# Kernel tuning notes

Measured on AMD Instinct MI355X. Metric: run time of the kernel, lower is better.

## Reference

```python
import jax, jax.numpy as jnp
import numpy as np
from jax import lax

EPS = 1e-6
NUM_BANDS = 128


def setup_inputs() -> dict:
    key = jax.random.key(0)
    kx, = jax.random.split(key, 1)
    B, C, F, T = 32, 1, NUM_BANDS, 6000
    x = jax.random.uniform(kx, (B, C, F, T), dtype=jnp.float32)  # nonneg spectrogram energies
    # parameters per band, initialized as in PCEN.__init__ (s=0.025, alpha=delta=r=1.0)
    log_s = jnp.full((F,), np.log(0.025), dtype=jnp.float32)
    log_alpha = jnp.zeros((F,), dtype=jnp.float32)
    log_delta = jnp.zeros((F,), dtype=jnp.float32)
    log_r = jnp.zeros((F,), dtype=jnp.float32)
    return {"x": x, "log_s": log_s, "log_alpha": log_alpha,
            "log_delta": log_delta, "log_r": log_r}


def _pcen(x, log_s, log_alpha, log_delta, log_r):
    # x: (B, C, bands, T)
    s = jnp.exp(log_s)  # (bands,)
    xt = jnp.moveaxis(x, -1, 0)  # (T, B, C, bands) time-major for the scan
    init = xt[0]  # init_smoother_from_data=True -> M_0 = X_0

    def step(m, xf):
        m_new = (1.0 - s) * m + s * xf
        return m_new, m_new

    _, ms = lax.scan(step, init, xt[1:])  # (T-1, B, C, bands)
    smoother = jnp.concatenate([init[None], ms], axis=0)  # (T, B, C, bands)
    smoother = jnp.moveaxis(smoother, 0, -1)  # (B, C, bands, T)

    alpha = jnp.exp(log_alpha)[:, None]  # (bands, 1)
    delta = jnp.exp(log_delta)[:, None]
    r = jnp.exp(log_r)[:, None]
    # (eps + M)^(-alpha) computed stably: exp(-alpha * (log eps + log1p(M/eps)))
    gain = jnp.exp(-alpha * (jnp.log(EPS) + jnp.log1p(smoother / EPS)))
    return (x * gain + delta) ** r - delta ** r


def reference(x, log_s, log_alpha, log_delta, log_r):
    return _pcen(x, log_s, log_alpha, log_delta, log_r)
```

## Files before the change

kernel.cpp:

```cpp
#include <hip/hip_runtime.h>

#define TLEN     6000
#define NV4      1500
#define CHUNK_V4 256
#define SUB_V4   64
#define NCHUNK   6
#define EPS      1e-6f
#define LN_EPS   (-13.815511f)
#define INV_EPS  1e6f

__device__ __forceinline__ float pcen_full(float xv, float M, float alpha,
                                           float delta, float r, float deltar) {
    float gain = __expf(-alpha * (LN_EPS + __logf(fmaf(M, INV_EPS, 1.0f))));
    return __powf(fmaf(xv, gain, delta), r) - deltar;
}

__device__ __forceinline__ float ipow6(float b, int e) {
    float r = 1.0f;
    #pragma unroll
    for (int i = 0; i < 6; ++i) {
        if (e & 1) r *= b;
        b *= b;
        e >>= 1;
    }
    return r;
}

template<bool PARTIAL>
__device__ __forceinline__ float chunk_compute(
    const float4 (&q)[4], const int cb, const int lane, const bool finit,
    const float s, const float oms, const float oms4, const float Apow4,
    const float A256, const bool triv,
    const float la, const float ld, const float lr,
    float Mc, float4* __restrict__ ob)
{
    float B[4];
    #pragma unroll
    for (int j = 0; j < 4; ++j) {
        const float c0 = (finit && j == 0 && lane == 0) ? 1.0f : s;
        float b = c0 * q[j].x;
        b = fmaf(oms, b, s * q[j].y);
        b = fmaf(oms, b, s * q[j].z);
        b = fmaf(oms, b, s * q[j].w);
        B[j] = b;
    }

    float S[4];
    #pragma unroll
    for (int j = 0; j < 4; ++j) S[j] = B[j];
    float w = oms4;
    #pragma unroll
    for (int off = 1; off < 64; off <<= 1) {
        #pragma unroll
        for (int j = 0; j < 4; ++j) {
            const float Sp = __shfl_up(S[j], off, 64);
            if (lane >= off) S[j] = fmaf(w, Sp, S[j]);
        }
        w *= w;
    }

    float Min[4];
    #pragma unroll
    for (int j = 0; j < 4; ++j) {
        const float Se = __shfl_up(S[j], 1, 64);
        const float Be = (lane == 0) ? 0.0f : Se;
        Min[j] = fmaf(Apow4, Mc, Be);
        Mc = fmaf(A256, Mc, __shfl(S[j], 63, 64));
    }

    if (triv) {
        #pragma unroll
        for (int j = 0; j < 4; ++j) {
            const int vi = cb + SUB_V4 * j + lane;
            if (!PARTIAL || vi < NV4) {
                const float c0 = (finit && j == 0 && lane == 0) ? 1.0f : s;
                float m = Min[j]; float4 o;
                m = fmaf(oms, m, c0 * q[j].x); o.x = q[j].x * __builtin_amdgcn_rcpf(m + EPS);
                m = fmaf(oms, m, s  * q[j].y); o.y = q[j].y * __builtin_amdgcn_rcpf(m + EPS);
                m = fmaf(oms, m, s  * q[j].z); o.z = q[j].z * __builtin_amdgcn_rcpf(m + EPS);
                m = fmaf(oms, m, s  * q[j].w); o.w = q[j].w * __builtin_amdgcn_rcpf(m + EPS);
                ob[vi] = o;
            }
        }
    } else {
        const float alpha  = __expf(la);
        const float delta  = __expf(ld);
        const float r      = __expf(lr);
        const float deltar = __powf(delta, lr == 0.0f ? 1.0f : r);
        #pragma unroll
        for (int j = 0; j < 4; ++j) {
            const int vi = cb + SUB_V4 * j + lane;
            if (!PARTIAL || vi < NV4) {
                const float c0 = (finit && j == 0 && lane == 0) ? 1.0f : s;
                float m = Min[j]; float4 o;
                m = fmaf(oms, m, c0 * q[j].x); o.x = pcen_full(q[j].x, m, alpha, delta, r, deltar);
                m = fmaf(oms, m, s  * q[j].y); o.y = pcen_full(q[j].y, m, alpha, delta, r, deltar);
                m = fmaf(oms, m, s  * q[j].z); o.z = pcen_full(q[j].z, m, alpha, delta, r, deltar);
                m = fmaf(oms, m, s  * q[j].w); o.w = pcen_full(q[j].w, m, alpha, delta, r, deltar);
                ob[vi] = o;
            }
        }
    }
    return Mc;
}

__global__ __launch_bounds__(256, 4) void pcen_kernel(
    const float* __restrict__ x,
    const float* __restrict__ log_s,
    const float* __restrict__ log_alpha,
    const float* __restrict__ log_delta,
    const float* __restrict__ log_r,
    float* __restrict__ out,
    int num_series, int F)
{
    const int g    = (int)((blockIdx.x * blockDim.x + threadIdx.x) >> 6);
    const int lane = (int)(threadIdx.x & 63);
    if (g >= num_series) return;
    const int series = g;
    const int f      = series % F;

    const float la = log_alpha[f], ld = log_delta[f], lr = log_r[f];
    const bool  triv = (la == 0.0f) && (ld == 0.0f) && (lr == 0.0f);

    const float s    = __expf(log_s[f]);
    const float oms  = 1.0f - s;
    const float oms2 = oms * oms;
    const float oms4 = oms2 * oms2;

    float A256 = oms4;
    #pragma unroll
    for (int i = 0; i < 6; ++i) A256 *= A256;

    const float Apow4 = ipow6(oms4, lane);

    const float4* __restrict__ xb = (const float4*)(x + (size_t)series * TLEN);
    float4* __restrict__ ob       = (float4*)(out + (size_t)series * TLEN);

    float4 b0[4], b1[4], b2[4];

    #pragma unroll
    for (int j = 0; j < 4; ++j) b0[j] = xb[0 * CHUNK_V4 + SUB_V4 * j + lane];
    #pragma unroll
    for (int j = 0; j < 4; ++j) b1[j] = xb[1 * CHUNK_V4 + SUB_V4 * j + lane];

    float Mc = 0.0f;

    #pragma unroll
    for (int j = 0; j < 4; ++j) b2[j] = xb[2 * CHUNK_V4 + SUB_V4 * j + lane];
    Mc = chunk_compute<false>(b0, 0 * CHUNK_V4, lane, true,
                              s, oms, oms4, Apow4, A256, triv, la, ld, lr, Mc, ob);

    #pragma unroll
    for (int j = 0; j < 4; ++j) b0[j] = xb[3 * CHUNK_V4 + SUB_V4 * j + lane];
    Mc = chunk_compute<false>(b1, 1 * CHUNK_V4, lane, false,
                              s, oms, oms4, Apow4, A256, triv, la, ld, lr, Mc, ob);

    #pragma unroll
    for (int j = 0; j < 4; ++j) b1[j] = xb[4 * CHUNK_V4 + SUB_V4 * j + lane];
    Mc = chunk_compute<false>(b2, 2 * CHUNK_V4, lane, false,
                              s, oms, oms4, Apow4, A256, triv, la, ld, lr, Mc, ob);

    #pragma unroll
    for (int j = 0; j < 4; ++j) {
        const int vi = 5 * CHUNK_V4 + SUB_V4 * j + lane;
        b2[j] = (vi < NV4) ? xb[vi] : make_float4(0.f, 0.f, 0.f, 0.f);
    }
    Mc = chunk_compute<false>(b0, 3 * CHUNK_V4, lane, false,
                              s, oms, oms4, Apow4, A256, triv, la, ld, lr, Mc, ob);

    Mc = chunk_compute<false>(b1, 4 * CHUNK_V4, lane, false,
                              s, oms, oms4, Apow4, A256, triv, la, ld, lr, Mc, ob);

    chunk_compute<true>(b2, 5 * CHUNK_V4, lane, false,
                        s, oms, oms4, Apow4, A256, triv, la, ld, lr, Mc, ob);
}

extern "C" void kernel_launch(void* const* d_in, const int* in_sizes, int n_in,
                              void* d_out, int out_size, void* d_ws, size_t ws_size,
                              hipStream_t stream) {
    const float* x         = (const float*)d_in[0];
    const float* log_s     = (const float*)d_in[1];
    const float* log_alpha = (const float*)d_in[2];
    const float* log_delta = (const float*)d_in[3];
    const float* log_r     = (const float*)d_in[4];
    float* out             = (float*)d_out;

    const int F = in_sizes[1];
    const int num_series = in_sizes[0] / TLEN;
    const int num_waves  = num_series;
    const int num_threads = num_waves * 64;
    const int grid = (num_threads + 255) / 256;

    pcen_kernel<<<grid, 256, 0, stream>>>(x, log_s, log_alpha, log_delta, log_r,
                                          out, num_series, F);
}
```

Baseline: 191.5 us.

## Widen scan chunks to 8 sub-blocks with double-buffered prefetch across 3 chunks

Each wave now scans chunks of 512 float4 values (8 independent sub-scans) instead of 256, so each series takes 3 chunk steps instead of 6. Buffering drops from triple to double. The carry between sub-blocks is computed as a short serial prefix over the chunk totals, and the shuffle that builds each lane's entry value is moved into the output loop. More independent shuffle chains per step should hide latency and cut the number of serial carry hops, but prefetch depth falls and register pressure rises; an explicit waves_per_eu attribute is added to hold occupancy.

```diff
diff --git a/kernel.cpp b/kernel.cpp
--- a/kernel.cpp
+++ b/kernel.cpp
@@ -1,13 +1,13 @@
 #include <hip/hip_runtime.h>
 
-#define TLEN     6000
-#define NV4      1500
-#define CHUNK_V4 256
-#define SUB_V4   64
-#define NCHUNK   6
-#define EPS      1e-6f
-#define LN_EPS   (-13.815511f)
-#define INV_EPS  1e6f
+#define TLEN    6000
+#define NV4     1500
+#define CH_V4   512
+#define SUB_V4  64
+#define NSUB    8
+#define EPS     1e-6f
+#define LN_EPS  (-13.815511f)
+#define INV_EPS 1e6f
 
 __device__ __forceinline__ float pcen_full(float xv, float M, float alpha,
                                            float delta, float r, float deltar) {
@@ -28,53 +28,52 @@
 
 template<bool PARTIAL>
 __device__ __forceinline__ float chunk_compute(
-    const float4 (&q)[4], const int cb, const int lane, const bool finit,
+    const float4 (&q)[NSUB], const int cb, const int lane, const bool finit,
     const float s, const float oms, const float oms4, const float Apow4,
     const float A256, const bool triv,
     const float la, const float ld, const float lr,
     float Mc, float4* __restrict__ ob)
 {
-    float B[4];
+    float S[NSUB];
     #pragma unroll
-    for (int j = 0; j < 4; ++j) {
+    for (int j = 0; j < NSUB; ++j) {
         const float c0 = (finit && j == 0 && lane == 0) ? 1.0f : s;
         float b = c0 * q[j].x;
         b = fmaf(oms, b, s * q[j].y);
         b = fmaf(oms, b, s * q[j].z);
         b = fmaf(oms, b, s * q[j].w);
-        B[j] = b;
+        S[j] = b;
     }
 
-    float S[4];
-    #pragma unroll
-    for (int j = 0; j < 4; ++j) S[j] = B[j];
     float w = oms4;
     #pragma unroll
     for (int off = 1; off < 64; off <<= 1) {
         #pragma unroll
-        for (int j = 0; j < 4; ++j) {
+        for (int j = 0; j < NSUB; ++j) {
             const float Sp = __shfl_up(S[j], off, 64);
             if (lane >= off) S[j] = fmaf(w, Sp, S[j]);
         }
         w *= w;
     }
 
-    float Min[4];
+    float T[NSUB];
     #pragma unroll
-    for (int j = 0; j < 4; ++j) {
-        const float Se = __shfl_up(S[j], 1, 64);
-        const float Be = (lane == 0) ? 0.0f : Se;
-        Min[j] = fmaf(Apow4, Mc, Be);
-        Mc = fmaf(A256, Mc, __shfl(S[j], 63, 64));
-    }
+    for (int j = 0; j < NSUB; ++j) T[j] = __shfl(S[j], 63, 64);
+    float P[NSUB + 1];
+    P[0] = Mc;
+    #pragma unroll
+    for (int j = 0; j < NSUB; ++j) P[j + 1] = fmaf(A256, P[j], T[j]);
 
     if (triv) {
         #pragma unroll
-        for (int j = 0; j < 4; ++j) {
+        for (int j = 0; j < NSUB; ++j) {
             const int vi = cb + SUB_V4 * j + lane;
+            const float Se = __shfl_up(S[j], 1, 64);
+            const float Be = (lane == 0) ? 0.0f : Se;
+            float m = fmaf(Apow4, P[j], Be);
             if (!PARTIAL || vi < NV4) {
                 const float c0 = (finit && j == 0 && lane == 0) ? 1.0f : s;
-                float m = Min[j]; float4 o;
+                float4 o;
                 m = fmaf(oms, m, c0 * q[j].x); o.x = q[j].x * __builtin_amdgcn_rcpf(m + EPS);
                 m = fmaf(oms, m, s  * q[j].y); o.y = q[j].y * __builtin_amdgcn_rcpf(m + EPS);
                 m = fmaf(oms, m, s  * q[j].z); o.z = q[j].z * __builtin_amdgcn_rcpf(m + EPS);
@@ -88,11 +87,14 @@
         const float r      = __expf(lr);
         const float deltar = __powf(delta, lr == 0.0f ? 1.0f : r);
         #pragma unroll
-        for (int j = 0; j < 4; ++j) {
+        for (int j = 0; j < NSUB; ++j) {
             const int vi = cb + SUB_V4 * j + lane;
+            const float Se = __shfl_up(S[j], 1, 64);
+            const float Be = (lane == 0) ? 0.0f : Se;
+            float m = fmaf(Apow4, P[j], Be);
             if (!PARTIAL || vi < NV4) {
                 const float c0 = (finit && j == 0 && lane == 0) ? 1.0f : s;
-                float m = Min[j]; float4 o;
+                float4 o;
                 m = fmaf(oms, m, c0 * q[j].x); o.x = pcen_full(q[j].x, m, alpha, delta, r, deltar);
                 m = fmaf(oms, m, s  * q[j].y); o.y = pcen_full(q[j].y, m, alpha, delta, r, deltar);
                 m = fmaf(oms, m, s  * q[j].z); o.z = pcen_full(q[j].z, m, alpha, delta, r, deltar);
@@ -101,10 +103,12 @@
             }
         }
     }
-    return Mc;
+    return P[NSUB];
 }
 
-__global__ __launch_bounds__(256, 4) void pcen_kernel(
+__global__ __launch_bounds__(256)
+__attribute__((amdgpu_waves_per_eu(4, 4)))
+void pcen_kernel(
     const float* __restrict__ x,
     const float* __restrict__ log_s,
     const float* __restrict__ log_alpha,
@@ -116,8 +120,7 @@
     const int g    = (int)((blockIdx.x * blockDim.x + threadIdx.x) >> 6);
     const int lane = (int)(threadIdx.x & 63);
     if (g >= num_series) return;
-    const int series = g;
-    const int f      = series % F;
+    const int f = g % F;
 
     const float la = log_alpha[f], ld = log_delta[f], lr = log_r[f];
     const bool  triv = (la == 0.0f) && (ld == 0.0f) && (lr == 0.0f);
@@ -133,45 +136,31 @@
 
     const float Apow4 = ipow6(oms4, lane);
 
-    const float4* __restrict__ xb = (const float4*)(x + (size_t)series * TLEN);
-    float4* __restrict__ ob       = (float4*)(out + (size_t)series * TLEN);
+    const float4* __restrict__ xb = (const float4*)(x + (size_t)g * TLEN);
+    float4* __restrict__ ob       = (float4*)(out + (size_t)g * TLEN);
 
-    float4 b0[4], b1[4], b2[4];
+    float4 bufA[NSUB], bufB[NSUB];
 
     #pragma unroll
-    for (int j = 0; j < 4; ++j) b0[j] = xb[0 * CHUNK_V4 + SUB_V4 * j + lane];
+    for (int j = 0; j < NSUB; ++j) bufA[j] = xb[SUB_V4 * j + lane];
     #pragma unroll
-    for (int j = 0; j < 4; ++j) b1[j] = xb[1 * CHUNK_V4 + SUB_V4 * j + lane];
+    for (int j = 0; j < NSUB; ++j) bufB[j] = xb[CH_V4 + SUB_V4 * j + lane];
 
     float Mc = 0.0f;
 
-    #pragma unroll
-    for (int j = 0; j < 4; ++j) b2[j] = xb[2 * CHUNK_V4 + SUB_V4 * j + lane];
-    Mc = chunk_compute<false>(b0, 0 * CHUNK_V4, lane, true,
+    Mc = chunk_compute<false>(bufA, 0, lane, true,
                               s, oms, oms4, Apow4, A256, triv, la, ld, lr, Mc, ob);
 
     #pragma unroll
-    for (int j = 0; j < 4; ++j) b0[j] = xb[3 * CHUNK_V4 + SUB_V4 * j + lane];
-    Mc = chunk_compute<false>(b1, 1 * CHUNK_V4, lane, false,
+    for (int j = 0; j < NSUB; ++j) {
+        const int vi = 2 * CH_V4 + SUB_V4 * j + lane;
+        bufA[j] = (vi < NV4) ? xb[vi] : make_float4(0.f, 0.f, 0.f, 0.f);
+    }
+
+    Mc = chunk_compute<false>(bufB, CH_V4, lane, false,
                               s, oms, oms4, Apow4, A256, triv, la, ld, lr, Mc, ob);
 
-    #pragma unroll
-    for (int j = 0; j < 4; ++j) b1[j] = xb[4 * CHUNK_V4 + SUB_V4 * j + lane];
-    Mc = chunk_compute<false>(b2, 2 * CHUNK_V4, lane, false,
-                              s, oms, oms4, Apow4, A256, triv, la, ld, lr, Mc, ob);
-
-    #pragma unroll
-    for (int j = 0; j < 4; ++j) {
-        const int vi = 5 * CHUNK_V4 + SUB_V4 * j + lane;
-        b2[j] = (vi < NV4) ? xb[vi] : make_float4(0.f, 0.f, 0.f, 0.f);
-    }
-    Mc = chunk_compute<false>(b0, 3 * CHUNK_V4, lane, false,
-                              s, oms, oms4, Apow4, A256, triv, la, ld, lr, Mc, ob);
-
-    Mc = chunk_compute<false>(b1, 4 * CHUNK_V4, lane, false,
-                              s, oms, oms4, Apow4, A256, triv, la, ld, lr, Mc, ob);
-
-    chunk_compute<true>(b2, 5 * CHUNK_V4, lane, false,
+    chunk_compute<true>(bufA, 2 * CH_V4, lane, false,
                         s, oms, oms4, Apow4, A256, triv, la, ld, lr, Mc, ob);
 }
 
```

Result: slower. 207.1 us (+8.1%).
